# Kernel tuning notes

Hardware: AMD Instinct MI355X
Metric: run time of the kernel (lower is better)

The kernel has to match this reference:

```python
import jax, jax.numpy as jnp
import numpy as np

BINS = 10
ALPHA = 0.75
MOMENTUM = 0.9
MU = 1.0


def setup_inputs() -> dict:
    key = jax.random.key(0)
    k1, k2 = jax.random.split(key)
    N = 8388608
    # angles in degrees, [0, 360)
    pred = jax.random.uniform(k1, (N, 1), dtype=jnp.float32) * 360.0
    target = jax.random.uniform(k2, (N, 1), dtype=jnp.float32) * 360.0
    acc_sum = jnp.zeros((BINS,), dtype=jnp.float32)  # module state, fresh
    return {"pred": pred, "target": target, "acc_sum": acc_sum}


def reference(pred, target, acc_sum):
    # angular difference, wrapped to [0, 180], normalized to [0, 1]
    diff = jnp.abs(pred - target)
    diff = jnp.minimum(diff, 360.0 - diff)
    g = diff / 180.0
    total = jnp.asarray(g.size, dtype=g.dtype)

    # bin index: edges are i/bins, last edge padded by 1e-6 so g==1.0 -> last bin
    idx = jnp.clip(jnp.floor(g * BINS).astype(jnp.int32), 0, BINS - 1)

    # single-pass histogram (replaces per-bin masked sums + .item() syncs)
    counts = jnp.zeros((BINS,), dtype=g.dtype).at[idx.reshape(-1)].add(1.0)
    nonempty = counts > 0
    acc_new = jnp.where(nonempty, MOMENTUM * acc_sum + (1.0 - MOMENTUM) * counts, acc_sum)
    n = jnp.sum(nonempty).astype(g.dtype)
    n_safe = jnp.maximum(n, 1.0)

    # per-bin weight, gathered per element (weights are constants in torch: built from .item())
    w_bin = jnp.where(acc_new > 0, total / (n_safe * jnp.maximum(acc_new, 1e-30)), 0.0)
    weights = jnp.where(n > 0, w_bin[idx], jnp.ones_like(g))
    weights = jax.lax.stop_gradient(weights ** ALPHA)

    # smooth L1 with beta = mu
    d = pred - target
    ad = jnp.abs(d)
    loss = jnp.where(ad < MU, 0.5 * d * d / MU, ad - 0.5 * MU)
    return jnp.mean(loss * weights)
```

## Files before the change

### kernel.cpp

```cpp
#include <hip/hip_runtime.h>

#define BINS 10
#define BLOCK 256
#define GRID 2048

__global__ __launch_bounds__(BLOCK) void ghmr_histo_kernel(
    const float* __restrict__ pred,
    const float* __restrict__ target,
    float* __restrict__ part_cnt,
    float* __restrict__ part_sum,
    int n)
{
    float c[BINS];
    float s[BINS];
#pragma unroll
    for (int b = 0; b < BINS; ++b) { c[b] = 0.0f; s[b] = 0.0f; }

    const int tid    = blockIdx.x * BLOCK + threadIdx.x;
    const int stride = gridDim.x * BLOCK;
    const int n4     = n >> 2;

    const float4* p4 = reinterpret_cast<const float4*>(pred);
    const float4* t4 = reinterpret_cast<const float4*>(target);

    for (int i = tid; i < n4; i += stride) {
        float4 p = p4[i];
        float4 t = t4[i];
        float pe[4] = {p.x, p.y, p.z, p.w};
        float te[4] = {t.x, t.y, t.z, t.w};
#pragma unroll
        for (int k = 0; k < 4; ++k) {
            float d  = pe[k] - te[k];
            float ad = fabsf(d);
            float wd = fminf(ad, 360.0f - ad);
            float g  = wd / 180.0f;
            int idx  = (int)floorf(g * 10.0f);
            idx = min(max(idx, 0), BINS - 1);
            float ls = (ad < 1.0f) ? (0.5f * d * d) : (ad - 0.5f);
#pragma unroll
            for (int b = 0; b < BINS; ++b) {
                float mf = (idx == b) ? 1.0f : 0.0f;
                c[b] += mf;
                s[b] = fmaf(mf, ls, s[b]);
            }
        }
    }
    for (int i = (n4 << 2) + tid; i < n; i += stride) {
        float d  = pred[i] - target[i];
        float ad = fabsf(d);
        float wd = fminf(ad, 360.0f - ad);
        float g  = wd / 180.0f;
        int idx  = (int)floorf(g * 10.0f);
        idx = min(max(idx, 0), BINS - 1);
        float ls = (ad < 1.0f) ? (0.5f * d * d) : (ad - 0.5f);
#pragma unroll
        for (int b = 0; b < BINS; ++b) {
            float mf = (idx == b) ? 1.0f : 0.0f;
            c[b] += mf;
            s[b] = fmaf(mf, ls, s[b]);
        }
    }

#pragma unroll
    for (int b = 0; b < BINS; ++b) {
#pragma unroll
        for (int off = 32; off > 0; off >>= 1) {
            c[b] += __shfl_down(c[b], off, 64);
            s[b] += __shfl_down(s[b], off, 64);
        }
    }

    __shared__ float lc[4][BINS];
    __shared__ float ls_[4][BINS];
    const int wave = threadIdx.x >> 6;
    const int lane = threadIdx.x & 63;
    if (lane == 0) {
#pragma unroll
        for (int b = 0; b < BINS; ++b) { lc[wave][b] = c[b]; ls_[wave][b] = s[b]; }
    }
    __syncthreads();
    if (threadIdx.x < BINS) {
        const int b = threadIdx.x;
        float cb = lc[0][b] + lc[1][b] + lc[2][b] + lc[3][b];
        float sb = ls_[0][b] + ls_[1][b] + ls_[2][b] + ls_[3][b];
        part_cnt[b * gridDim.x + blockIdx.x] = cb;
        part_sum[b * gridDim.x + blockIdx.x] = sb;
    }
}

__global__ __launch_bounds__(64 * BINS) void ghmr_reduce_final(
    const float* __restrict__ part_cnt,
    const float* __restrict__ part_sum,
    const float* __restrict__ acc_sum,
    float* __restrict__ out,
    float total, int nblk)
{
    const int wave = threadIdx.x >> 6;
    const int lane = threadIdx.x & 63;

    float csum = 0.0f, ssum = 0.0f;
    const float* pc = part_cnt + wave * nblk;
    const float* ps = part_sum + wave * nblk;
    for (int i = lane; i < nblk; i += 64) { csum += pc[i]; ssum += ps[i]; }
#pragma unroll
    for (int off = 32; off > 0; off >>= 1) {
        csum += __shfl_down(csum, off, 64);
        ssum += __shfl_down(ssum, off, 64);
    }

    __shared__ float C[BINS];
    __shared__ float S[BINS];
    if (lane == 0) { C[wave] = csum; S[wave] = ssum; }
    __syncthreads();

    if (threadIdx.x == 0) {
        float acc_new[BINS];
        int n_nonempty = 0;
#pragma unroll
        for (int b = 0; b < BINS; ++b) {
            float cnt = C[b];
            bool ne = (cnt > 0.0f);
            acc_new[b] = ne ? (0.9f * acc_sum[b] + 0.1f * cnt) : acc_sum[b];
            n_nonempty += ne ? 1 : 0;
        }
        float n_safe = fmaxf((float)n_nonempty, 1.0f);

        double weighted = 0.0;
        double plain    = 0.0;
#pragma unroll
        for (int b = 0; b < BINS; ++b) {
            float wb = (acc_new[b] > 0.0f)
                           ? (total / (n_safe * fmaxf(acc_new[b], 1e-30f)))
                           : 0.0f;
            float wp = powf(wb, 0.75f);
            weighted += (double)S[b] * (double)wp;
            plain    += (double)S[b];
        }
        double res = ((n_nonempty > 0) ? weighted : plain) / (double)total;
        out[0] = (float)res;
    }
}

extern "C" void kernel_launch(void* const* d_in, const int* in_sizes, int n_in,
                              void* d_out, int out_size, void* d_ws, size_t ws_size,
                              hipStream_t stream) {
    const float* pred    = (const float*)d_in[0];
    const float* target  = (const float*)d_in[1];
    const float* acc_sum = (const float*)d_in[2];
    float* out = (float*)d_out;
    const int n = in_sizes[0];

    int nblk = GRID;
    size_t need = (size_t)2 * BINS * (size_t)nblk * sizeof(float);
    if (ws_size < need) {
        nblk = (int)(ws_size / ((size_t)2 * BINS * sizeof(float)));
        if (nblk < 1) nblk = 1;
    }

    float* part_cnt = (float*)d_ws;
    float* part_sum = part_cnt + (size_t)BINS * nblk;

    ghmr_histo_kernel<<<nblk, BLOCK, 0, stream>>>(pred, target, part_cnt, part_sum, n);
    ghmr_reduce_final<<<1, 64 * BINS, 0, stream>>>(part_cnt, part_sum, acc_sum, out,
                                                   (float)n, nblk);
}
```

Measured before the change: 114.0 us.

## Use per-thread shared-memory histogram instead of register one-hot bin accumulation

Replaces the per-element loop over all 10 bins (one-hot compare and FMA into register arrays) with a private per-thread slot in LDS, indexed directly by bin, plus a block-level tree reduction at the end. The grid is halved, partials are packed as float2, and the divide and floor are replaced by a reciprocal multiply and truncation. This removes about 20 ALU ops per element in exchange for an LDS read-modify-write, 20KB of shared memory per block, and fewer blocks to hide memory latency.

```diff
diff --git a/kernel.cpp b/kernel.cpp
--- a/kernel.cpp
+++ b/kernel.cpp
@@ -2,21 +2,22 @@
 
 #define BINS 10
 #define BLOCK 256
-#define GRID 2048
+#define GRID 1024
 
 __global__ __launch_bounds__(BLOCK) void ghmr_histo_kernel(
     const float* __restrict__ pred,
     const float* __restrict__ target,
-    float* __restrict__ part_cnt,
-    float* __restrict__ part_sum,
+    float2* __restrict__ part,
     int n)
 {
-    float c[BINS];
-    float s[BINS];
+    __shared__ float2 h[BINS][BLOCK];
+    const int t = threadIdx.x;
 #pragma unroll
-    for (int b = 0; b < BINS; ++b) { c[b] = 0.0f; s[b] = 0.0f; }
+    for (int b = 0; b < BINS; ++b) h[b][t] = make_float2(0.0f, 0.0f);
+    __syncthreads();
 
-    const int tid    = blockIdx.x * BLOCK + threadIdx.x;
+    const float INV180 = 1.0f / 180.0f;
+    const int tid    = blockIdx.x * BLOCK + t;
     const int stride = gridDim.x * BLOCK;
     const int n4     = n >> 2;
 
@@ -25,83 +26,76 @@
 
     for (int i = tid; i < n4; i += stride) {
         float4 p = p4[i];
-        float4 t = t4[i];
+        float4 q = t4[i];
         float pe[4] = {p.x, p.y, p.z, p.w};
-        float te[4] = {t.x, t.y, t.z, t.w};
+        float te[4] = {q.x, q.y, q.z, q.w};
 #pragma unroll
         for (int k = 0; k < 4; ++k) {
             float d  = pe[k] - te[k];
             float ad = fabsf(d);
             float wd = fminf(ad, 360.0f - ad);
-            float g  = wd / 180.0f;
-            int idx  = (int)floorf(g * 10.0f);
+            float g  = wd * INV180;
+            float gg = g * 10.0f;
+            int idx  = (int)gg;
             idx = min(max(idx, 0), BINS - 1);
             float ls = (ad < 1.0f) ? (0.5f * d * d) : (ad - 0.5f);
-#pragma unroll
-            for (int b = 0; b < BINS; ++b) {
-                float mf = (idx == b) ? 1.0f : 0.0f;
-                c[b] += mf;
-                s[b] = fmaf(mf, ls, s[b]);
-            }
+            float2 v = h[idx][t];
+            v.x += 1.0f;
+            v.y += ls;
+            h[idx][t] = v;
         }
     }
     for (int i = (n4 << 2) + tid; i < n; i += stride) {
         float d  = pred[i] - target[i];
         float ad = fabsf(d);
         float wd = fminf(ad, 360.0f - ad);
-        float g  = wd / 180.0f;
-        int idx  = (int)floorf(g * 10.0f);
+        float g  = wd * INV180;
+        float gg = g * 10.0f;
+        int idx  = (int)gg;
         idx = min(max(idx, 0), BINS - 1);
         float ls = (ad < 1.0f) ? (0.5f * d * d) : (ad - 0.5f);
-#pragma unroll
-        for (int b = 0; b < BINS; ++b) {
-            float mf = (idx == b) ? 1.0f : 0.0f;
-            c[b] += mf;
-            s[b] = fmaf(mf, ls, s[b]);
-        }
-    }
-
-#pragma unroll
-    for (int b = 0; b < BINS; ++b) {
-#pragma unroll
-        for (int off = 32; off > 0; off >>= 1) {
-            c[b] += __shfl_down(c[b], off, 64);
-            s[b] += __shfl_down(s[b], off, 64);
-        }
-    }
-
-    __shared__ float lc[4][BINS];
-    __shared__ float ls_[4][BINS];
-    const int wave = threadIdx.x >> 6;
-    const int lane = threadIdx.x & 63;
-    if (lane == 0) {
-#pragma unroll
-        for (int b = 0; b < BINS; ++b) { lc[wave][b] = c[b]; ls_[wave][b] = s[b]; }
+        float2 v = h[idx][t];
+        v.x += 1.0f;
+        v.y += ls;
+        h[idx][t] = v;
     }
     __syncthreads();
-    if (threadIdx.x < BINS) {
-        const int b = threadIdx.x;
-        float cb = lc[0][b] + lc[1][b] + lc[2][b] + lc[3][b];
-        float sb = ls_[0][b] + ls_[1][b] + ls_[2][b] + ls_[3][b];
-        part_cnt[b * gridDim.x + blockIdx.x] = cb;
-        part_sum[b * gridDim.x + blockIdx.x] = sb;
+
+    if (t < 16 * BINS) {
+        const int r = t >> 4;
+        const int j = t & 15;
+        float c = 0.0f, s = 0.0f;
+#pragma unroll
+        for (int k = 0; k < 16; ++k) {
+            float2 v = h[r][j + 16 * k];
+            c += v.x;
+            s += v.y;
+        }
+#pragma unroll
+        for (int off = 8; off > 0; off >>= 1) {
+            c += __shfl_down(c, off, 16);
+            s += __shfl_down(s, off, 16);
+        }
+        if (j == 0) part[r * gridDim.x + blockIdx.x] = make_float2(c, s);
     }
 }
 
 __global__ __launch_bounds__(64 * BINS) void ghmr_reduce_final(
-    const float* __restrict__ part_cnt,
-    const float* __restrict__ part_sum,
-    const float* __restrict__ acc_sum,
+    const float2* __restrict__ part,
+    const float*  __restrict__ acc_sum,
     float* __restrict__ out,
     float total, int nblk)
 {
-    const int wave = threadIdx.x >> 6;
+    const int w    = threadIdx.x >> 6;
     const int lane = threadIdx.x & 63;
 
     float csum = 0.0f, ssum = 0.0f;
-    const float* pc = part_cnt + wave * nblk;
-    const float* ps = part_sum + wave * nblk;
-    for (int i = lane; i < nblk; i += 64) { csum += pc[i]; ssum += ps[i]; }
+    const float2* pw = part + (size_t)w * nblk;
+    for (int i = lane; i < nblk; i += 64) {
+        float2 v = pw[i];
+        csum += v.x;
+        ssum += v.y;
+    }
 #pragma unroll
     for (int off = 32; off > 0; off >>= 1) {
         csum += __shfl_down(csum, off, 64);
@@ -110,7 +104,7 @@
 
     __shared__ float C[BINS];
     __shared__ float S[BINS];
-    if (lane == 0) { C[wave] = csum; S[wave] = ssum; }
+    if (lane == 0) { C[w] = csum; S[w] = ssum; }
     __syncthreads();
 
     if (threadIdx.x == 0) {
@@ -151,16 +145,14 @@
     const int n = in_sizes[0];
 
     int nblk = GRID;
-    size_t need = (size_t)2 * BINS * (size_t)nblk * sizeof(float);
+    size_t need = (size_t)BINS * (size_t)nblk * sizeof(float2);
     if (ws_size < need) {
-        nblk = (int)(ws_size / ((size_t)2 * BINS * sizeof(float)));
+        nblk = (int)(ws_size / ((size_t)BINS * sizeof(float2)));
         if (nblk < 1) nblk = 1;
     }
 
-    float* part_cnt = (float*)d_ws;
-    float* part_sum = part_cnt + (size_t)BINS * nblk;
+    float2* part = (float2*)d_ws;
 
-    ghmr_histo_kernel<<<nblk, BLOCK, 0, stream>>>(pred, target, part_cnt, part_sum, n);
-    ghmr_reduce_final<<<1, 64 * BINS, 0, stream>>>(part_cnt, part_sum, acc_sum, out,
-                                                   (float)n, nblk);
+    ghmr_histo_kernel<<<nblk, BLOCK, 0, stream>>>(pred, target, part, n);
+    ghmr_reduce_final<<<1, 64 * BINS, 0, stream>>>(part, acc_sum, out, (float)n, nblk);
 }
```

After: 102.8 us (median of 2 runs). 9.9% less time.
